# Kernel optimization log

Hardware: AMD Instinct MI355X
Metric: run time of the kernel (lower is better)

Reference implementation:

```python
import jax, jax.numpy as jnp
import numpy as np

WIN = 2048      # window_size / conv kernel size
HOP = 128       # hop_size / conv stride
SR = 22050
N_MELS = 128
N_FREQ = WIN // 2 + 1  # 1025


def _fourier_weights(window_size=WIN):
    # Faithful to get_fourier_weights_for_mel (hanning=True)
    frec = np.linspace(-window_size // 2, 0, window_size // 2 + 1)
    time = np.linspace(0, window_size - 1, window_size)
    hann = np.hanning(window_size)
    cos_f = np.array([np.cos(2 * np.pi * f * time / window_size) for f in frec])
    sin_f = np.array([np.sin(2 * np.pi * f * time / window_size) for f in frec])
    return cos_f[::-1] * hann, sin_f[::-1] * hann


def _hz_to_mel(f):
    # librosa slaney mel scale
    f = np.atleast_1d(np.asarray(f, dtype=np.float64))
    f_sp = 200.0 / 3.0
    mels = f / f_sp
    min_log_hz = 1000.0
    min_log_mel = min_log_hz / f_sp
    logstep = np.log(6.4) / 27.0
    log_t = f >= min_log_hz
    mels[log_t] = min_log_mel + np.log(f[log_t] / min_log_hz) / logstep
    return mels


def _mel_to_hz(m):
    m = np.atleast_1d(np.asarray(m, dtype=np.float64))
    f_sp = 200.0 / 3.0
    freqs = f_sp * m
    min_log_hz = 1000.0
    min_log_mel = min_log_hz / f_sp
    logstep = np.log(6.4) / 27.0
    log_t = m >= min_log_mel
    freqs[log_t] = min_log_hz * np.exp(logstep * (m[log_t] - min_log_mel))
    return freqs


def _mel_filterbank(sr=SR, n_fft=WIN, n_mels=N_MELS, fmin=0.0, fmax=None):
    # Faithful to librosa.filters.mel (htk=False, norm='slaney')
    if fmax is None:
        fmax = sr / 2.0
    fftfreqs = np.linspace(0.0, sr / 2.0, n_fft // 2 + 1)
    mel_pts = np.linspace(_hz_to_mel(fmin)[0], _hz_to_mel(fmax)[0], n_mels + 2)
    mel_f = _mel_to_hz(mel_pts)                       # [n_mels+2]
    fdiff = np.diff(mel_f)
    ramps = mel_f[:, None] - fftfreqs[None, :]
    lower = -ramps[:-2] / fdiff[:-1, None]
    upper = ramps[2:] / fdiff[1:, None]
    weights = np.maximum(0.0, np.minimum(lower, upper))  # [n_mels, n_freq]
    enorm = 2.0 / (mel_f[2:n_mels + 2] - mel_f[:n_mels])
    return weights * enorm[:, None]


def setup_inputs() -> dict:
    key = jax.random.key(0)
    B, T = 8, 2048 + 128 * 5151  # -> n_frames = 5152
    x = jax.random.normal(key, (B, 1, T), dtype=jnp.float32)
    cos_np, sin_np = _fourier_weights()
    return {
        "x": x,
        "cos_w": jnp.asarray(np.ascontiguousarray(cos_np), dtype=jnp.float32),  # [1025, 2048]
        "sin_w": jnp.asarray(np.ascontiguousarray(sin_np), dtype=jnp.float32),  # [1025, 2048]
        "mel_w": jnp.asarray(_mel_filterbank(), dtype=jnp.float32),             # [128, 1025]
    }


def reference(x, cos_w, sin_w, mel_w):
    # x: [B, 1, T]
    T = x.shape[-1]
    n_frames = (T - WIN) // HOP + 1
    idx = jnp.arange(n_frames)[:, None] * HOP + jnp.arange(WIN)[None, :]
    frames = x[:, 0, :][:, idx]
    c = jnp.einsum('btw,fw->bft', frames, cos_w)     # [B, N_FREQ, n_frames]
    s = jnp.einsum('btw,fw->bft', frames, sin_w)
    power = c * c + s * s                            # power spectrum
    mel = jnp.einsum('mf,bft->bmt', mel_w, power)    # 1x1 conv == channel matmul
    return mel  # in_db=False default
```

## Files before the change

### kernel.cpp

```cpp
#include <hip/hip_runtime.h>
#include <stdint.h>

#define NB 8
#define TLEN 661376
#define NFR 5152
#define NFREQ 1025
#define NMEL 128
#define NFRP 5376
#define OUT_BT (NMEL * NFR)

typedef unsigned int u32;
typedef float f32x4 __attribute__((ext_vector_type(4)));
typedef short s16x8 __attribute__((ext_vector_type(8)));
typedef u32 u32x4 __attribute__((ext_vector_type(4)));

__device__ __forceinline__ u32 f2bf(float f) {
  u32 u = __float_as_uint(f);
  return (u + 0x7FFFu + ((u >> 16) & 1u)) >> 16;
}
__device__ __forceinline__ u32 packbf(float a, float b) {
  return f2bf(a) | (f2bf(b) << 16);
}
__device__ __forceinline__ void bar_lgkm() {
  asm volatile("s_waitcnt lgkmcnt(0)" ::: "memory");
  __builtin_amdgcn_s_barrier();
  __builtin_amdgcn_sched_barrier(0);
}

#define WCAN_BYTES 9437184
#define MCAN_OFF   9437184
#define MCAN_BYTES 294912
#define P_OFF      9732096
#define P_ROWB     2304
#define TIER1_NEED 108822528ULL
#define TIER2_NEED 61636608ULL
#define TIER3_NEED 42762240ULL

__global__ void prep_wcan(const float* __restrict__ cw, const float* __restrict__ sw,
                          char* __restrict__ wg) {
  int id = blockIdx.x * 256 + threadIdx.x;
  int jp = id & 3, l15 = (id >> 2) & 15, l4 = (id >> 6) & 3;
  int fr = (id >> 8) & 15, k = (id >> 12) & 63, g = id >> 18;
  if (g >= 9) return;
  int freq = g * 128 + (fr >> 1) * 16 + l15;
  const float* src = (fr & 1) ? sw : cw;
  u32 pk = 0;
  if (freq < NFREQ) {
    int smp = k * 32 + l4 * 8 + jp * 2;
    pk = packbf(src[(size_t)freq * 2048 + smp], src[(size_t)freq * 2048 + smp + 1]);
  }
  *(u32*)(wg + (size_t)id * 4) = pk;
}

__global__ void prep_mcan(const float* __restrict__ mw, char* __restrict__ mg) {
  int id = blockIdx.x * 256 + threadIdx.x;
  if (id >= 73728) return;
  int jp = id & 3, l15 = (id >> 2) & 15, l4 = (id >> 6) & 3;
  int fr = (id >> 8) & 7, ks = id >> 11;
  int m = fr * 16 + l15;
  int f = ks * 32 + l4 * 8 + jp * 2;
  float v0 = (f < NFREQ) ? mw[(size_t)m * NFREQ + f] : 0.f;
  float v1 = (f + 1 < NFREQ) ? mw[(size_t)m * NFREQ + f + 1] : 0.f;
  *(u32*)(mg + (size_t)id * 4) = packbf(v0, v1);
}

#define K1_X 69376
#define K1_LDS 102144
__global__ __launch_bounds__(512, 2) void k1_power(
    const float* __restrict__ x, const char* __restrict__ wg,
    char* __restrict__ P, int tstart, int tcap) {
  __shared__ __align__(16) char smem[K1_LDS];
  const int tid = threadIdx.x;
  const int lane = tid & 63, wid = tid >> 6;
  const int l15 = lane & 15, l4 = lane >> 4;
  const int fw = wid & 3, tw = wid >> 2;
  const int tb = blockIdx.x, g = blockIdx.y, b = blockIdx.z;
  const int t0 = tstart + tb * 256;

  {
    const float* xb = x + (size_t)b * TLEN;
    const int sbase = t0 * 128;
#pragma unroll
    for (int i = 0; i < 9; ++i) {
      int q = tid + i * 512;
      if (q < 4336) {
        int s0 = sbase + q * 8;
        u32 r0, r1, r2, r3;
        if (s0 + 8 <= TLEN) {
          f32x4 v0 = *(const f32x4*)(xb + s0);
          f32x4 v1 = *(const f32x4*)(xb + s0 + 4);
          r0 = packbf(v0[0], v0[1]); r1 = packbf(v0[2], v0[3]);
          r2 = packbf(v1[0], v1[1]); r3 = packbf(v1[2], v1[3]);
        } else {
          float e[8];
#pragma unroll
          for (int j = 0; j < 8; ++j) { int s = s0 + j; e[j] = (s < TLEN) ? xb[s] : 0.f; }
          r0 = packbf(e[0], e[1]); r1 = packbf(e[2], e[3]);
          r2 = packbf(e[4], e[5]); r3 = packbf(e[6], e[7]);
        }
        int lb = q * 16;
        *(u32x4*)(smem + (lb ^ (((lb >> 8) & 7) << 4))) = (u32x4){r0, r1, r2, r3};
      }
    }
  }

  f32x4 acc[4][8];
#pragma unroll
  for (int i = 0; i < 4; ++i)
#pragma unroll
    for (int j = 0; j < 8; ++j) acc[i][j] = (f32x4){0.f, 0.f, 0.f, 0.f};

  const char* wslab = wg + (size_t)g * (64 * 16384);
  u32x4 wr0 = *(const u32x4*)(wslab + tid * 16);
  u32x4 wr1 = *(const u32x4*)(wslab + tid * 16 + 8192);

  int bfbase[8], bfkey[8];
#pragma unroll
  for (int nt = 0; nt < 8; ++nt) {
    int lt = tw * 128 + nt * 16 + l15;
    bfbase[nt] = lt * 256 + l4 * 16;
    bfkey[nt] = lt & 7;
  }
  const int afoff = (fw * 4) * 1024 + l4 * 256 + l15 * 16;

  for (int k = 0; k < 64; ++k) {
    char* wb = smem + K1_X + (k & 1) * 16384;
    *(u32x4*)(wb + tid * 16) = wr0;
    *(u32x4*)(wb + tid * 16 + 8192) = wr1;
    bar_lgkm();
    if (k + 1 < 64) {
      const char* ns = wslab + (k + 1) * 16384;
      wr0 = *(const u32x4*)(ns + tid * 16);
      wr1 = *(const u32x4*)(ns + tid * 16 + 8192);
    }
    s16x8 af[4], bf[8];
#pragma unroll
    for (int m4 = 0; m4 < 4; ++m4)
      af[m4] = *(const s16x8*)(wb + afoff + m4 * 1024);
    const int kq = k >> 2;
#pragma unroll
    for (int nt = 0; nt < 8; ++nt) {
      int a = bfbase[nt] + k * 64;
      bf[nt] = *(const s16x8*)(smem + (a ^ (((bfkey[nt] + kq) & 7) << 4)));
    }
    __builtin_amdgcn_s_setprio(1);
#pragma unroll
    for (int m4 = 0; m4 < 4; ++m4)
#pragma unroll
      for (int nt = 0; nt < 8; ++nt)
        acc[m4][nt] = __builtin_amdgcn_mfma_f32_16x16x32_bf16(af[m4], bf[nt],
                                                              acc[m4][nt], 0, 0, 0);
    __builtin_amdgcn_s_setprio(0);
  }
  bar_lgkm();

  char* plds = smem + K1_X;
#pragma unroll
  for (int h = 0; h < 2; ++h) {
    if (tw == h) {
#pragma unroll
      for (int q = 0; q < 2; ++q)
#pragma unroll
        for (int nt = 0; nt < 8; ++nt) {
          f32x4 c = acc[q * 2][nt], s = acc[q * 2 + 1][nt];
          float p0 = c[0] * c[0] + s[0] * s[0];
          float p1 = c[1] * c[1] + s[1] * s[1];
          float p2 = c[2] * c[2] + s[2] * s[2];
          float p3 = c[3] * c[3] + s[3] * s[3];
          int lt = nt * 16 + l15;
          int fl = fw * 32 + q * 16 + l4 * 4;
          int a = lt * 256 + fl * 2;
          int sw = (lt & 7) << 4;
          *(u32*)(plds + (a ^ sw)) = packbf(p0, p1);
          *(u32*)(plds + ((a + 4) ^ sw)) = packbf(p2, p3);
        }
    }
    bar_lgkm();
#pragma unroll
    for (int i = 0; i < 4; ++i) {
      int lin = (tid + i * 512) * 16;
      u32x4 v = *(const u32x4*)(plds + (lin ^ (((lin >> 8) & 7) << 4)));
      int tc = tb * 256 + h * 128 + (lin >> 8);
      *(u32x4*)(P + ((size_t)b * tcap + tc) * P_ROWB + g * 256 + (lin & 255)) = v;
    }
    bar_lgkm();
  }
}

__global__ __launch_bounds__(256, 4) void k2_mel(
    const char* __restrict__ P, const char* __restrict__ mg,
    float* __restrict__ out, int tstart, int tcap) {
  __shared__ __align__(16) char sm[4096];
  const int tid = threadIdx.x;
  const int lane = tid & 63, wid = tid >> 6;
  const int l15 = lane & 15, l4 = lane >> 4;
  const int tb = blockIdx.x, b = blockIdx.y;
  const int tz = tb * 64;

  const int st_t = tid >> 2, st_fo = tid & 3;
  const char* prow = P + ((size_t)b * tcap + tz + st_t) * P_ROWB + st_fo * 16;

  f32x4 acc[2][4];
#pragma unroll
  for (int i = 0; i < 2; ++i)
#pragma unroll
    for (int j = 0; j < 4; ++j) acc[i][j] = (f32x4){0.f, 0.f, 0.f, 0.f};

  u32x4 pr = *(const u32x4*)prow;
  const int lw = (st_t * 64 + st_fo * 16) ^ ((st_t & 7) << 4);
  const int afo = l4 * 256 + l15 * 16;

  for (int ks = 0; ks < 36; ++ks) {
    *(u32x4*)(sm + lw) = pr;
    bar_lgkm();
    if (ks + 1 < 36) pr = *(const u32x4*)(prow + (ks + 1) * 64);
    s16x8 a0 = *(const s16x8*)(mg + (size_t)(ks * 8 + wid * 2) * 1024 + afo);
    s16x8 a1 = *(const s16x8*)(mg + (size_t)(ks * 8 + wid * 2 + 1) * 1024 + afo);
    s16x8 bf[4];
#pragma unroll
    for (int nt = 0; nt < 4; ++nt) {
      int a = ((nt * 16 + l15) * 64 + l4 * 16) ^ ((l15 & 7) << 4);
      bf[nt] = *(const s16x8*)(sm + a);
    }
#pragma unroll
    for (int nt = 0; nt < 4; ++nt) {
      acc[0][nt] = __builtin_amdgcn_mfma_f32_16x16x32_bf16(a0, bf[nt], acc[0][nt], 0, 0, 0);
      acc[1][nt] = __builtin_amdgcn_mfma_f32_16x16x32_bf16(a1, bf[nt], acc[1][nt], 0, 0, 0);
    }
    bar_lgkm();
  }

#pragma unroll
  for (int nt = 0; nt < 4; ++nt) {
    int t = tstart + tz + nt * 16 + l15;
    if (t < NFR) {
#pragma unroll
      for (int mf = 0; mf < 2; ++mf)
#pragma unroll
        for (int ii = 0; ii < 4; ++ii) {
          int m = wid * 32 + mf * 16 + l4 * 4 + ii;
          out[(size_t)b * OUT_BT + (size_t)m * NFR + t] = acc[mf][nt][ii];
        }
    }
  }
}

#define F_BT 96
#define F_NTT 54
#define F_NGRP 17
#define F_GI_TOT 1088
#define F_SLABB 8192
#define F_XSB 28416
#define F_XS_OFF 0
#define F_WL_OFF 28416
#define F_PL_OFF 36608
#define F_ML_OFF 48896
#define F_LDS_TOT 65280
#define F_WS_MG 8912896
#define F_WS_NEED 9191424
#define F_MLB 16384

__device__ __forceinline__ int f_swzW(int a) { return a ^ (((a >> 6) & 7) << 4); }
__device__ __forceinline__ int f_swzR(int a) { return a ^ (((a >> 7) & 7) << 4); }

__global__ void f_prep_w(const float* __restrict__ cw, const float* __restrict__ sw,
                         char* __restrict__ wg) {
  int id = blockIdx.x * 256 + threadIdx.x;
  int j = id & 15, r = (id >> 4) & 127, gi = id >> 11;
  if (gi >= F_GI_TOT) return;
  int g = gi >> 6, k0 = gi & 63;
  int c = r >> 5, r5 = r & 31;
  int f = g * 64 + c * 16 + (r5 & 15);
  const float* src = (r5 < 16) ? cw : sw;
  u32 pk = 0;
  if (f < NFREQ) {
    int k = k0 * 32 + j * 2;
    pk = packbf(src[(size_t)f * 2048 + k], src[(size_t)f * 2048 + k + 1]);
  }
  *(u32*)(wg + (size_t)gi * F_SLABB + r * 64 + j * 4) = pk;
}

__global__ void f_prep_mel(const float* __restrict__ mw, char* __restrict__ mg) {
  int id = blockIdx.x * 256 + threadIdx.x;
  int fp = id & 31, m = (id >> 5) & 127, g = id >> 12;
  if (g >= F_NGRP) return;
  int f = g * 64 + fp * 2;
  float v0 = (f < NFREQ) ? mw[m * NFREQ + f] : 0.f;
  float v1 = (f + 1 < NFREQ) ? mw[m * NFREQ + f + 1] : 0.f;
  int a = m * 128 + fp * 4;
  *(u32*)(mg + (size_t)g * F_MLB + (a ^ ((m & 7) << 4))) = packbf(v0, v1);
}

template <bool PRIM>
__global__ __launch_bounds__(512, 4) void f_mel_main(
    const float* __restrict__ x, const char* __restrict__ wg,
    const char* __restrict__ mg, const float* __restrict__ cw,
    const float* __restrict__ sw, const float* __restrict__ mw,
    float* __restrict__ out) {
  __shared__ __align__(16) char smem[F_LDS_TOT];
  const int tid = threadIdx.x;
  const int lane = tid & 63, wid = tid >> 6;
  const int l15 = lane & 15, l4 = lane >> 4;
  const int bid = blockIdx.x;
  const int b = bid / F_NTT, tt = bid - b * F_NTT;
  const int t0 = tt * F_BT;
  const int c2 = wid >> 1, jh = wid & 1;

  {
    const float* xb = x + (size_t)b * TLEN + (size_t)t0 * 128;
    const int qn = (TLEN - t0 * 128) >> 3;
    for (int it = 0; it < 4; ++it) {
      int q = tid + it * 512;
      if (q < F_XSB / 16) {
        u32 r0 = 0, r1 = 0, r2 = 0, r3 = 0;
        if (q < qn) {
          f32x4 v0 = *(const f32x4*)(xb + q * 8);
          f32x4 v1 = *(const f32x4*)(xb + q * 8 + 4);
          r0 = packbf(v0[0], v0[1]); r1 = packbf(v0[2], v0[3]);
          r2 = packbf(v1[0], v1[1]); r3 = packbf(v1[2], v1[3]);
        }
        int a = q * 16;
        int ph = a ^ ((((a >> 8) + t0) & 7) << 4);
        *(u32x4*)(smem + F_XS_OFF + ph) = (u32x4){r0, r1, r2, r3};
      }
    }
  }

  f32x4 acc[2][3];
  f32x4 mel[6];
#pragma unroll
  for (int i = 0; i < 2; ++i)
#pragma unroll
    for (int j = 0; j < 3; ++j) acc[i][j] = (f32x4){0.f, 0.f, 0.f, 0.f};
#pragma unroll
  for (int i = 0; i < 6; ++i) mel[i] = (f32x4){0.f, 0.f, 0.f, 0.f};

  u32x4 wr_p = {0, 0, 0, 0};
  f32x4 wf0 = {0, 0, 0, 0}, wf1 = {0, 0, 0, 0};
  const int wr_r = tid >> 2, wr_j = tid & 3;
  const int wr_c = wr_r >> 5, wr_r5 = wr_r & 31;

  auto loadW = [&](int gi) {
    if (PRIM) {
      wr_p = *(const u32x4*)(wg + (size_t)gi * F_SLABB + tid * 16);
    } else {
      int g = gi >> 6, k0 = gi & 63;
      int f = g * 64 + wr_c * 16 + (wr_r5 & 15);
      if (f < NFREQ) {
        const float* src = (wr_r5 < 16) ? cw : sw;
        const float* p = src + (size_t)f * 2048 + k0 * 32 + wr_j * 8;
        wf0 = *(const f32x4*)p;
        wf1 = *(const f32x4*)(p + 4);
      } else {
        wf0 = (f32x4){0, 0, 0, 0};
        wf1 = (f32x4){0, 0, 0, 0};
      }
    }
  };

  loadW(0);

  for (int gi = 0; gi < F_GI_TOT; ++gi) {
    const int g = gi >> 6, k0 = gi & 63;
    {
      int a = tid * 16;
      u32x4 v;
      if (PRIM) v = wr_p;
      else v = (u32x4){packbf(wf0[0], wf0[1]), packbf(wf0[2], wf0[3]),
                       packbf(wf1[0], wf1[1]), packbf(wf1[2], wf1[3])};
      *(u32x4*)(smem + F_WL_OFF + f_swzW(a)) = v;
    }
    if (k0 == 0) {
      for (int i = 0; i < 2; ++i) {
        int h = tid + i * 512;
        if (PRIM) {
          u32x4 v = *(const u32x4*)(mg + (size_t)g * F_MLB + h * 16);
          *(u32x4*)(smem + F_ML_OFF + h * 16) = v;
        } else {
          int m = h >> 3, part = h & 7;
          int f0 = g * 64 + part * 8;
          u32 w[4];
#pragma unroll
          for (int e = 0; e < 4; ++e) {
            int f = f0 + e * 2;
            float v0 = (f < NFREQ) ? mw[m * NFREQ + f] : 0.f;
            float v1 = (f + 1 < NFREQ) ? mw[m * NFREQ + f + 1] : 0.f;
            w[e] = packbf(v0, v1);
          }
          int a = m * 128 + part * 16;
          *(u32x4*)(smem + F_ML_OFF + (a ^ ((m & 7) << 4))) = (u32x4){w[0], w[1], w[2], w[3]};
        }
      }
    }
    __syncthreads();
    if (gi + 1 < F_GI_TOT) loadW(gi + 1);

    const int kb = l4 * 16;
    s16x8 bf[3], af[2];
    const int xkey = (k0 >> 2) + t0;
#pragma unroll
    for (int nt = 0; nt < 3; ++nt) {
      const int lt = jh * 48 + nt * 16 + l15;
      const int lb = lt * 256 + k0 * 64 + kb;
      bf[nt] = *(const s16x8*)(smem + F_XS_OFF + (lb ^ (((lt + xkey) & 7) << 4)));
    }
#pragma unroll
    for (int cs = 0; cs < 2; ++cs) {
      const int row = c2 * 32 + cs * 16 + l15;
      af[cs] = *(const s16x8*)(smem + F_WL_OFF + f_swzW(row * 64 + kb));
    }
#pragma unroll
    for (int cs = 0; cs < 2; ++cs)
#pragma unroll
      for (int nt = 0; nt < 3; ++nt)
        acc[cs][nt] = __builtin_amdgcn_mfma_f32_16x16x32_bf16(af[cs], bf[nt],
                                                              acc[cs][nt], 0, 0, 0);

    if (k0 == 63) {
#pragma unroll
      for (int nt = 0; nt < 3; ++nt) {
        f32x4 pc = acc[0][nt], ps = acc[1][nt];
        float p0 = pc[0] * pc[0] + ps[0] * ps[0];
        float p1 = pc[1] * pc[1] + ps[1] * ps[1];
        float p2 = pc[2] * pc[2] + ps[2] * ps[2];
        float p3 = pc[3] * pc[3] + ps[3] * ps[3];
        const int t = jh * 48 + nt * 16 + l15;
        const int a0 = t * 128 + c2 * 32 + l4 * 8;
        const int sw = (t & 7) << 4;
        *(u32*)(smem + F_PL_OFF + (a0 ^ sw)) = packbf(p0, p1);
        *(u32*)(smem + F_PL_OFF + ((a0 + 4) ^ sw)) = packbf(p2, p3);
      }
#pragma unroll
      for (int i = 0; i < 2; ++i)
#pragma unroll
        for (int j = 0; j < 3; ++j) acc[i][j] = (f32x4){0.f, 0.f, 0.f, 0.f};
      __syncthreads();

      const int mrow = wid * 16 + l15;
#pragma unroll
      for (int ks = 0; ks < 2; ++ks) {
        s16x8 a2 = *(const s16x8*)(smem + F_ML_OFF + f_swzR(mrow * 128 + ks * 64 + kb));
#pragma unroll
        for (int n2 = 0; n2 < 6; ++n2) {
          const int tr = n2 * 16 + l15;
          s16x8 b2 = *(const s16x8*)(smem + F_PL_OFF + f_swzR(tr * 128 + ks * 64 + kb));
          mel[n2] = __builtin_amdgcn_mfma_f32_16x16x32_bf16(a2, b2, mel[n2], 0, 0, 0);
        }
      }
    }
    __syncthreads();
  }

#pragma unroll
  for (int n2 = 0; n2 < 6; ++n2) {
    const int t = t0 + n2 * 16 + l15;
    if (t < NFR) {
#pragma unroll
      for (int ii = 0; ii < 4; ++ii) {
        const int m = wid * 16 + l4 * 4 + ii;
        out[(size_t)b * OUT_BT + (size_t)m * NFR + t] = mel[n2][ii];
      }
    }
  }
}

extern "C" void kernel_launch(void* const* d_in, const int* in_sizes, int n_in,
                              void* d_out, int out_size, void* d_ws, size_t ws_size,
                              hipStream_t stream) {
  if (n_in < 4) return;
  const float* x  = (const float*)d_in[0];
  const float* cw = (const float*)d_in[1];
  const float* sw = (const float*)d_in[2];
  const float* mw = (const float*)d_in[3];
  float* out = (float*)d_out;
  char* ws = (char*)d_ws;

  int nchunks = 0, tcap = 0;
  int cstart[3], ctb[3];
  if (d_ws && ws_size >= TIER1_NEED) {
    nchunks = 1; tcap = 5376;
    cstart[0] = 0; ctb[0] = 21;
  } else if (d_ws && ws_size >= TIER2_NEED) {
    nchunks = 2; tcap = 2816;
    cstart[0] = 0; ctb[0] = 11; cstart[1] = 2816; ctb[1] = 10;
  } else if (d_ws && ws_size >= TIER3_NEED) {
    nchunks = 3; tcap = 1792;
    cstart[0] = 0; ctb[0] = 7; cstart[1] = 1792; ctb[1] = 7;
    cstart[2] = 3584; ctb[2] = 7;
  }

  if (nchunks > 0) {
    char* wg = ws;
    char* mg = ws + MCAN_OFF;
    char* P  = ws + P_OFF;
    prep_wcan<<<9216, 256, 0, stream>>>(cw, sw, wg);
    prep_mcan<<<288, 256, 0, stream>>>(mw, mg);
    for (int c = 0; c < nchunks; ++c) {
      dim3 g1(ctb[c], 9, NB);
      k1_power<<<g1, 512, 0, stream>>>(x, wg, P, cstart[c], tcap);
      dim3 g2(ctb[c] * 4, NB);
      k2_mel<<<g2, 256, 0, stream>>>(P, mg, out, cstart[c], tcap);
    }
    return;
  }

  const bool prim = (d_ws != nullptr) && (ws_size >= (size_t)F_WS_NEED);
  if (prim) {
    f_prep_w<<<F_GI_TOT * 2048 / 256, 256, 0, stream>>>(cw, sw, ws);
    f_prep_mel<<<F_NGRP * 4096 / 256, 256, 0, stream>>>(mw, ws + F_WS_MG);
    f_mel_main<true><<<NB * F_NTT, 512, 0, stream>>>(x, ws, ws + F_WS_MG,
                                                     cw, sw, mw, out);
  } else {
    f_mel_main<false><<<NB * F_NTT, 512, 0, stream>>>(x, nullptr, nullptr,
                                                      cw, sw, mw, out);
  }
}
```

Measured before the change: 439.8 us.

## Use triple-buffered LDS ring for DFT weights with register prefetch of operands

Replaces the double-buffered weight staging in the power kernel with a three-slot LDS ring and a prologue that preloads two slabs. Fragments for step k+1 are read into registers right after step k's MFMAs are issued, and the global load for step k+3 is issued one iteration earlier. The aim is to hide LDS read latency and global load latency behind MFMA work. In exchange, LDS use grows by 16 KB per block, which with two 512-thread blocks per CU may come close to the LDS limit and reduce occupancy.

```diff
diff --git a/kernel.cpp b/kernel.cpp
--- a/kernel.cpp
+++ b/kernel.cpp
@@ -65,7 +65,7 @@
 }
 
 #define K1_X 69376
-#define K1_LDS 102144
+#define K1_LDS 118528
 __global__ __launch_bounds__(512, 2) void k1_power(
     const float* __restrict__ x, const char* __restrict__ wg,
     char* __restrict__ P, int tstart, int tcap) {
@@ -111,8 +111,7 @@
     for (int j = 0; j < 8; ++j) acc[i][j] = (f32x4){0.f, 0.f, 0.f, 0.f};
 
   const char* wslab = wg + (size_t)g * (64 * 16384);
-  u32x4 wr0 = *(const u32x4*)(wslab + tid * 16);
-  u32x4 wr1 = *(const u32x4*)(wslab + tid * 16 + 8192);
+  char* ring = smem + K1_X;
 
   int bfbase[8], bfkey[8];
 #pragma unroll
@@ -123,26 +122,30 @@
   }
   const int afoff = (fw * 4) * 1024 + l4 * 256 + l15 * 16;
 
+  {
+    u32x4 a0 = *(const u32x4*)(wslab + tid * 16);
+    u32x4 a1 = *(const u32x4*)(wslab + tid * 16 + 8192);
+    u32x4 b0 = *(const u32x4*)(wslab + 16384 + tid * 16);
+    u32x4 b1 = *(const u32x4*)(wslab + 16384 + tid * 16 + 8192);
+    *(u32x4*)(ring + tid * 16) = a0;
+    *(u32x4*)(ring + tid * 16 + 8192) = a1;
+    *(u32x4*)(ring + 16384 + tid * 16) = b0;
+    *(u32x4*)(ring + 16384 + tid * 16 + 8192) = b1;
+  }
+  u32x4 wr0 = *(const u32x4*)(wslab + 2 * 16384 + tid * 16);
+  u32x4 wr1 = *(const u32x4*)(wslab + 2 * 16384 + tid * 16 + 8192);
+  bar_lgkm();
+
+  s16x8 af[4], bf[8];
+#pragma unroll
+  for (int m4 = 0; m4 < 4; ++m4)
+    af[m4] = *(const s16x8*)(ring + afoff + m4 * 1024);
+#pragma unroll
+  for (int nt = 0; nt < 8; ++nt)
+    bf[nt] = *(const s16x8*)(smem + (bfbase[nt] ^ ((bfkey[nt] & 7) << 4)));
+
+  int rd_n = 16384, wr_n = 32768;
   for (int k = 0; k < 64; ++k) {
-    char* wb = smem + K1_X + (k & 1) * 16384;
-    *(u32x4*)(wb + tid * 16) = wr0;
-    *(u32x4*)(wb + tid * 16 + 8192) = wr1;
-    bar_lgkm();
-    if (k + 1 < 64) {
-      const char* ns = wslab + (k + 1) * 16384;
-      wr0 = *(const u32x4*)(ns + tid * 16);
-      wr1 = *(const u32x4*)(ns + tid * 16 + 8192);
-    }
-    s16x8 af[4], bf[8];
-#pragma unroll
-    for (int m4 = 0; m4 < 4; ++m4)
-      af[m4] = *(const s16x8*)(wb + afoff + m4 * 1024);
-    const int kq = k >> 2;
-#pragma unroll
-    for (int nt = 0; nt < 8; ++nt) {
-      int a = bfbase[nt] + k * 64;
-      bf[nt] = *(const s16x8*)(smem + (a ^ (((bfkey[nt] + kq) & 7) << 4)));
-    }
     __builtin_amdgcn_s_setprio(1);
 #pragma unroll
     for (int m4 = 0; m4 < 4; ++m4)
@@ -151,8 +154,33 @@
         acc[m4][nt] = __builtin_amdgcn_mfma_f32_16x16x32_bf16(af[m4], bf[nt],
                                                               acc[m4][nt], 0, 0, 0);
     __builtin_amdgcn_s_setprio(0);
-  }
-  bar_lgkm();
+
+    if (k + 1 < 64) {
+      const char* rb = ring + rd_n;
+#pragma unroll
+      for (int m4 = 0; m4 < 4; ++m4)
+        af[m4] = *(const s16x8*)(rb + afoff + m4 * 1024);
+      const int kn = k + 1, kq = kn >> 2;
+#pragma unroll
+      for (int nt = 0; nt < 8; ++nt) {
+        int a = bfbase[nt] + kn * 64;
+        bf[nt] = *(const s16x8*)(smem + (a ^ (((bfkey[nt] + kq) & 7) << 4)));
+      }
+    }
+    if (k + 2 < 64) {
+      char* wb = ring + wr_n;
+      *(u32x4*)(wb + tid * 16) = wr0;
+      *(u32x4*)(wb + tid * 16 + 8192) = wr1;
+    }
+    if (k + 3 < 64) {
+      const char* ns = wslab + (k + 3) * 16384;
+      wr0 = *(const u32x4*)(ns + tid * 16);
+      wr1 = *(const u32x4*)(ns + tid * 16 + 8192);
+    }
+    rd_n += 16384; if (rd_n == 49152) rd_n = 0;
+    wr_n += 16384; if (wr_n == 49152) wr_n = 0;
+    bar_lgkm();
+  }
 
   char* plds = smem + K1_X;
 #pragma unroll
```

After: 440.2 us. No clear change (+0.1%).
